# Kernel tuning notes

Hardware: AMD Instinct MI355X
Metric: run time of the kernel (lower is better)

## Reference

```python
import jax, jax.numpy as jnp
import numpy as np

B, L, I, O = 65536, 16, 256, 256


def setup_inputs() -> dict:
    key = jax.random.key(0)
    k1, k2, k3, k4 = jax.random.split(key, 4)
    lookups = jax.random.uniform(k1, (B, L), dtype=jnp.float32)
    values = jax.random.normal(k2, (B, I), dtype=jnp.float32)
    # glorot-style scale for the weight bank
    weights_lookup = jax.random.normal(k3, (L, I, O), dtype=jnp.float32) * (1.0 / np.sqrt(I))
    bias_lookup = jnp.zeros((L, O), dtype=jnp.float32)
    return {"lookups": lookups, "values": values,
            "weights_lookup": weights_lookup, "bias_lookup": bias_lookup}


def reference(lookups, values, weights_lookup, bias_lookup):
    # tf.einsum('...i,...l,lio->...o') with bias einsum('...l,lo->...o'),
    # activation = 'linear' (identity).
    # Efficient contraction order: per-token routed values (b,l,i) is avoided by
    # contracting values with the weight bank per expert, then combining with
    # routing weights — equivalent math, single einsum lets XLA pick the order.
    weighted = jnp.einsum('bi,bl,lio->bo', values, lookups, weights_lookup)
    biases = jnp.einsum('bl,lo->bo', lookups, bias_lookup)
    return weighted + biases
```

## Files before the change

kernel.cpp:

```cpp
#include <hip/hip_runtime.h>
#include <hip/hip_fp16.h>
#include <stdint.h>


#define B_TOK 65536
#define L_DIM 16
#define I_DIM 256
#define O_DIM 256
#define BM    256
#define THREADS 512

#define AOFF  65536
#define LKOFF 98304
#define LKS   20

typedef __attribute__((ext_vector_type(8))) _Float16 f16x8;
typedef __attribute__((ext_vector_type(4))) float f32x4;
typedef __attribute__((address_space(3))) void      lds_void_t;
typedef const __attribute__((address_space(1))) void gbl_void_t;

static __device__ __forceinline__ f16x8 scale8(f16x8 a, __half2 s) {
    union { f16x8 v; __half2 h[4]; } u; u.v = a;
#pragma unroll
    for (int q = 0; q < 4; ++q) u.h[q] = __hmul2(u.h[q], s);
    return u.v;
}

__global__ void prep_w(const float* __restrict__ W, const float* __restrict__ bias,
                       unsigned short* __restrict__ ws) {
    const int t  = blockIdx.x;
    const int o  = blockIdx.y * 32 + (threadIdx.x & 31);
    const int cp = threadIdx.x >> 5;
    const int c  = cp ^ (o & 7);
    uint32_t p[4];
    if (t < 64) {
        const int l = t & 15, ibase = (t >> 4) * 64;
        const float* src = W + ((size_t)l * I_DIM + ibase + c * 8) * O_DIM + o;
#pragma unroll
        for (int jp = 0; jp < 4; ++jp) {
            float a = src[(size_t)(2 * jp) * O_DIM];
            float b = src[(size_t)(2 * jp + 1) * O_DIM];
            p[jp] = __builtin_bit_cast(uint32_t, __floats2half2_rn(a, b));
        }
    } else if (c < 2) {
#pragma unroll
        for (int jp = 0; jp < 4; ++jp) {
            int kk = c * 8 + 2 * jp;
            float a = bias[(size_t)kk * O_DIM + o];
            float b = bias[(size_t)(kk + 1) * O_DIM + o];
            p[jp] = __builtin_bit_cast(uint32_t, __floats2half2_rn(a, b));
        }
    } else {
        p[0] = p[1] = p[2] = p[3] = 0u;
    }
    uint4 q = {p[0], p[1], p[2], p[3]};
    *(uint4*)((char*)ws + (size_t)t * 32768 + o * 128 + cp * 16) = q;
}

__launch_bounds__(THREADS, 2)
__global__ void md_gemm(const float* __restrict__ lookups,
                        const float* __restrict__ values,
                        const unsigned short* __restrict__ Wst,
                        float* __restrict__ out) {
    __shared__ char smem[118784];

    const int tid  = threadIdx.x;
    const int wid  = tid >> 6;
    const int lane = tid & 63;
    const int row0 = blockIdx.x * BM;

    const int r = tid >> 1;
    const int h = tid & 1;

    const int wm   = wid >> 2;
    const int wn   = wid & 3;
    const int arow = wm * 128 + (lane & 15);
    const int bcol = wn * 64  + (lane & 15);
    const int kkl  = (lane >> 4) * 8;

    f32x4 acc[8][4];
#pragma unroll
    for (int m = 0; m < 8; ++m)
#pragma unroll
        for (int n = 0; n < 4; ++n) acc[m][n] = (f32x4){0.f, 0.f, 0.f, 0.f};

    auto stageB = [&](int kt, int nb) {
        const char* src = (const char*)Wst + (size_t)kt * 32768 + wid * 1024 + lane * 16;
        char* dst = smem + nb * 32768 + wid * 1024;
#pragma unroll
        for (int s = 0; s < 4; ++s)
            __builtin_amdgcn_global_load_lds((gbl_void_t*)(src + s * 8192),
                                             (lds_void_t*)(dst + s * 8192), 16, 0, 0);
    };

    {
        const float4* lp = (const float4*)(lookups + (size_t)(row0 + r) * L_DIM + h * 8);
        float4 f0 = lp[0], f1 = lp[1];
        float* dst = (float*)(smem + LKOFF) + r * LKS + h * 8;
        *(float4*)dst = f0;
        *(float4*)(dst + 4) = f1;
    }
    stageB(0, 0);

    const float* lkp = (const float*)(smem + LKOFF);

    for (int cc = 0; cc < 4; ++cc) {
        {
            const float4* vp = (const float4*)(values + (size_t)(row0 + r) * I_DIM
                                               + cc * 64 + h * 32);
            uint32_t p[16];
#pragma unroll
            for (int j = 0; j < 8; ++j) {
                float4 f = vp[j];
                p[2 * j]     = __builtin_bit_cast(uint32_t, __floats2half2_rn(f.x, f.y));
                p[2 * j + 1] = __builtin_bit_cast(uint32_t, __floats2half2_rn(f.z, f.w));
            }
            char* ab = smem + AOFF;
#pragma unroll
            for (int w = 0; w < 4; ++w) {
                uint4 q = {p[4 * w], p[4 * w + 1], p[4 * w + 2], p[4 * w + 3]};
                *(uint4*)(ab + ((r * 128 + h * 64 + w * 16) ^ ((r & 7) << 4))) = q;
            }
        }
        __syncthreads();

        f16x8 afk0[8];
#pragma unroll
        for (int mt = 0; mt < 8; ++mt) {
            int row = arow + mt * 16;
            afk0[mt] = *(f16x8*)(smem + AOFF + ((row * 128 + kkl * 2) ^ ((row & 7) << 4)));
        }

        for (int l = 0; l < 16; ++l) {
            const int kt = cc * 16 + l;
            if (l != 0) {
                asm volatile("s_waitcnt vmcnt(0)\n\ts_barrier" ::: "memory");
            }
            __half2 lk2[8];
#pragma unroll
            for (int mt = 0; mt < 8; ++mt)
                lk2[mt] = __float2half2_rn(lkp[(arow + mt * 16) * LKS + l]);

            char* bbase = smem + (kt & 1) * 32768;
            f16x8 bfr[4];
#pragma unroll
            for (int nt = 0; nt < 4; ++nt) {
                int o = bcol + nt * 16;
                bfr[nt] = *(f16x8*)(bbase + ((o * 128 + kkl * 2) ^ ((o & 7) << 4)));
            }
#pragma unroll
            for (int mt = 0; mt < 8; ++mt) {
                f16x8 a = scale8(afk0[mt], lk2[mt]);
#pragma unroll
                for (int nt = 0; nt < 4; ++nt)
                    acc[mt][nt] = __builtin_amdgcn_mfma_f32_16x16x32_f16(
                        a, bfr[nt], acc[mt][nt], 0, 0, 0);
            }
#pragma unroll
            for (int nt = 0; nt < 4; ++nt) {
                int o = bcol + nt * 16;
                bfr[nt] = *(f16x8*)(bbase + ((o * 128 + 64 + kkl * 2) ^ ((o & 7) << 4)));
            }
#pragma unroll
            for (int mt = 0; mt < 8; ++mt) {
                int row = arow + mt * 16;
                f16x8 a1 = *(f16x8*)(smem + AOFF
                                     + ((row * 128 + 64 + kkl * 2) ^ ((row & 7) << 4)));
                a1 = scale8(a1, lk2[mt]);
#pragma unroll
                for (int nt = 0; nt < 4; ++nt)
                    acc[mt][nt] = __builtin_amdgcn_mfma_f32_16x16x32_f16(
                        a1, bfr[nt], acc[mt][nt], 0, 0, 0);
            }
            stageB(kt + 1, (kt + 1) & 1);
        }
        asm volatile("s_barrier" ::: "memory");
    }

    {
        uint32_t p[16];
#pragma unroll
        for (int j = 0; j < 16; ++j) p[j] = 0u;
        if (h == 0) {
            const float* lr = lkp + r * LKS;
#pragma unroll
            for (int j = 0; j < 8; ++j)
                p[j] = __builtin_bit_cast(uint32_t, __floats2half2_rn(lr[2 * j], lr[2 * j + 1]));
        }
        char* ab = smem + AOFF;
#pragma unroll
        for (int w = 0; w < 4; ++w) {
            uint4 q = {p[4 * w], p[4 * w + 1], p[4 * w + 2], p[4 * w + 3]};
            *(uint4*)(ab + ((r * 128 + h * 64 + w * 16) ^ ((r & 7) << 4))) = q;
        }
    }
    __syncthreads();
    {
        f16x8 bfr[4];
#pragma unroll
        for (int nt = 0; nt < 4; ++nt) {
            int o = bcol + nt * 16;
            bfr[nt] = *(f16x8*)(smem + ((o * 128 + kkl * 2) ^ ((o & 7) << 4)));
        }
#pragma unroll
        for (int mt = 0; mt < 8; ++mt) {
            int row = arow + mt * 16;
            f16x8 a0 = *(f16x8*)(smem + AOFF + ((row * 128 + kkl * 2) ^ ((row & 7) << 4)));
#pragma unroll
            for (int nt = 0; nt < 4; ++nt)
                acc[mt][nt] = __builtin_amdgcn_mfma_f32_16x16x32_f16(
                    a0, bfr[nt], acc[mt][nt], 0, 0, 0);
        }
    }

    const int orow = row0 + wm * 128 + (lane >> 4) * 4;
    const int ocol = wn * 64 + (lane & 15);
#pragma unroll
    for (int mt = 0; mt < 8; ++mt)
#pragma unroll
        for (int nt = 0; nt < 4; ++nt) {
#pragma unroll
            for (int j = 0; j < 4; ++j)
                out[(size_t)(orow + mt * 16 + j) * O_DIM + ocol + nt * 16] = acc[mt][nt][j];
        }
}

extern "C" void kernel_launch(void* const* d_in, const int* in_sizes, int n_in,
                              void* d_out, int out_size, void* d_ws, size_t ws_size,
                              hipStream_t stream) {
    const float* lookups = (const float*)d_in[0];
    const float* values  = (const float*)d_in[1];
    const float* W       = (const float*)d_in[2];
    const float* bias    = (const float*)d_in[3];
    unsigned short* Wst  = (unsigned short*)d_ws;

    prep_w<<<dim3(65, 8), dim3(256), 0, stream>>>(W, bias, Wst);
    md_gemm<<<dim3(B_TOK / BM), dim3(THREADS), 0, stream>>>(lookups, values, Wst,
                                                            (float*)d_out);
}
```

Before: 233.3 us.

## Triple-buffer weight tiles and interleave split async loads with MFMA phases

Replaces the double-buffered weight staging with a three-slot ring fetched two tiles ahead. Each tile's four async global-to-LDS loads are spread across four MFMA sub-phases, bracketed by barriers and raised wave priority. The per-chunk outer loop is flattened into one 64-step loop that reloads the activation slice at chunk boundaries, and the next routing scalar is prefetched into registers. The lookup row stride changes to 17 to reduce LDS bank conflicts. The cost is more LDS and more barriers per iteration, which may add synchronisation overhead.

```diff
diff --git a/kernel.cpp b/kernel.cpp
--- a/kernel.cpp
+++ b/kernel.cpp
@@ -10,14 +10,18 @@
 #define BM    256
 #define THREADS 512
 
-#define AOFF  65536
-#define LKOFF 98304
-#define LKS   20
+#define BOFS(i) ((i) * 32768)
+#define AOFF    98304
+#define LKOFF   131072
+#define LKS     17
 
 typedef __attribute__((ext_vector_type(8))) _Float16 f16x8;
 typedef __attribute__((ext_vector_type(4))) float f32x4;
 typedef __attribute__((address_space(3))) void      lds_void_t;
 typedef const __attribute__((address_space(1))) void gbl_void_t;
+
+#define SBAR  __builtin_amdgcn_s_barrier()
+#define SCHED __builtin_amdgcn_sched_barrier(0)
 
 static __device__ __forceinline__ f16x8 scale8(f16x8 a, __half2 s) {
     union { f16x8 v; __half2 h[4]; } u; u.v = a;
@@ -62,7 +66,7 @@
                         const float* __restrict__ values,
                         const unsigned short* __restrict__ Wst,
                         float* __restrict__ out) {
-    __shared__ char smem[118784];
+    __shared__ char smem[148480];
 
     const int tid  = threadIdx.x;
     const int wid  = tid >> 6;
@@ -78,139 +82,211 @@
     const int bcol = wn * 64  + (lane & 15);
     const int kkl  = (lane >> 4) * 8;
 
+    float* lkp = (float*)(smem + LKOFF);
+
     f32x4 acc[8][4];
 #pragma unroll
     for (int m = 0; m < 8; ++m)
 #pragma unroll
         for (int n = 0; n < 4; ++n) acc[m][n] = (f32x4){0.f, 0.f, 0.f, 0.f};
 
-    auto stageB = [&](int kt, int nb) {
-        const char* src = (const char*)Wst + (size_t)kt * 32768 + wid * 1024 + lane * 16;
-        char* dst = smem + nb * 32768 + wid * 1024;
-#pragma unroll
-        for (int s = 0; s < 4; ++s)
-            __builtin_amdgcn_global_load_lds((gbl_void_t*)(src + s * 8192),
-                                             (lds_void_t*)(dst + s * 8192), 16, 0, 0);
+    auto stage1 = [&](int g, int tb, int s) {
+        const char* src = (const char*)Wst + (size_t)g * 32768 + wid * 1024
+                          + s * 8192 + lane * 16;
+        char* dst = smem + BOFS(tb) + wid * 1024 + s * 8192;
+        __builtin_amdgcn_global_load_lds((gbl_void_t*)src, (lds_void_t*)dst, 16, 0, 0);
+    };
+
+    auto stageA = [&](int cc) {
+        const float4* vp = (const float4*)(values + (size_t)(row0 + r) * I_DIM
+                                           + cc * 64 + h * 32);
+        uint32_t p[16];
+#pragma unroll
+        for (int j = 0; j < 8; ++j) {
+            float4 f = vp[j];
+            p[2 * j]     = __builtin_bit_cast(uint32_t, __floats2half2_rn(f.x, f.y));
+            p[2 * j + 1] = __builtin_bit_cast(uint32_t, __floats2half2_rn(f.z, f.w));
+        }
+        char* ab = smem + AOFF;
+#pragma unroll
+        for (int w = 0; w < 4; ++w) {
+            uint4 q = {p[4 * w], p[4 * w + 1], p[4 * w + 2], p[4 * w + 3]};
+            *(uint4*)(ab + ((r * 128 + h * 64 + w * 16) ^ ((r & 7) << 4))) = q;
+        }
+    };
+
+    auto stageA_bias = [&]() {
+        uint32_t p[16];
+#pragma unroll
+        for (int j = 0; j < 16; ++j) p[j] = 0u;
+        if (h == 0) {
+            const float* lr = lkp + r * LKS;
+#pragma unroll
+            for (int j = 0; j < 8; ++j)
+                p[j] = __builtin_bit_cast(uint32_t,
+                        __floats2half2_rn(lr[2 * j], lr[2 * j + 1]));
+        }
+        char* ab = smem + AOFF;
+#pragma unroll
+        for (int w = 0; w < 4; ++w) {
+            uint4 q = {p[4 * w], p[4 * w + 1], p[4 * w + 2], p[4 * w + 3]};
+            *(uint4*)(ab + ((r * 128 + h * 64 + w * 16) ^ ((r & 7) << 4))) = q;
+        }
     };
 
     {
         const float4* lp = (const float4*)(lookups + (size_t)(row0 + r) * L_DIM + h * 8);
         float4 f0 = lp[0], f1 = lp[1];
-        float* dst = (float*)(smem + LKOFF) + r * LKS + h * 8;
-        *(float4*)dst = f0;
-        *(float4*)(dst + 4) = f1;
-    }
-    stageB(0, 0);
-
-    const float* lkp = (const float*)(smem + LKOFF);
-
-    for (int cc = 0; cc < 4; ++cc) {
+        float* dst = lkp + r * LKS + h * 8;
+        dst[0] = f0.x; dst[1] = f0.y; dst[2] = f0.z; dst[3] = f0.w;
+        dst[4] = f1.x; dst[5] = f1.y; dst[6] = f1.z; dst[7] = f1.w;
+    }
+#pragma unroll
+    for (int s = 0; s < 4; ++s) stage1(0, 0, s);
+#pragma unroll
+    for (int s = 0; s < 4; ++s) stage1(1, 1, s);
+    stageA(0);
+    __syncthreads();
+
+    f16x8 afk0[8];
+#pragma unroll
+    for (int mt = 0; mt < 8; ++mt) {
+        int row = arow + mt * 16;
+        afk0[mt] = *(f16x8*)(smem + AOFF + ((row * 128 + kkl * 2) ^ ((row & 7) << 4)));
+    }
+    float lknf[8];
+#pragma unroll
+    for (int mt = 0; mt < 8; ++mt) lknf[mt] = lkp[(arow + mt * 16) * LKS];
+
+    int bi = 0;
+    for (int kt = 0; kt < 64; ++kt) {
+        const int  tb       = (kt + 2) % 3;
+        const bool boundary = (kt & 15) == 15;
+        char* bbase = smem + BOFS(bi);
+
+        __half2 lk2[8];
+#pragma unroll
+        for (int mt = 0; mt < 8; ++mt) lk2[mt] = __float2half2_rn(lknf[mt]);
+
+        f16x8 bfr[4];
+#pragma unroll
+        for (int nt = 0; nt < 4; ++nt) {
+            int o = bcol + nt * 16;
+            bfr[nt] = *(f16x8*)(bbase + ((o * 128 + kkl * 2) ^ ((o & 7) << 4)));
+        }
+        if (kt <= 62) stage1(kt + 2, tb, 0);
+        SBAR; SCHED;
+        __builtin_amdgcn_s_setprio(1);
+#pragma unroll
+        for (int m = 0; m < 4; ++m) {
+            f16x8 a = scale8(afk0[m], lk2[m]);
+#pragma unroll
+            for (int nt = 0; nt < 4; ++nt)
+                acc[m][nt] = __builtin_amdgcn_mfma_f32_16x16x32_f16(a, bfr[nt],
+                                                                    acc[m][nt], 0, 0, 0);
+        }
+        __builtin_amdgcn_s_setprio(0);
+        SCHED; SBAR;
+
+        f16x8 a1lo[4];
+#pragma unroll
+        for (int m = 0; m < 4; ++m) {
+            int row = arow + m * 16;
+            a1lo[m] = *(f16x8*)(smem + AOFF
+                                + ((row * 128 + 64 + kkl * 2) ^ ((row & 7) << 4)));
+        }
+        if (kt <= 62) stage1(kt + 2, tb, 1);
+        SBAR; SCHED;
+        __builtin_amdgcn_s_setprio(1);
+#pragma unroll
+        for (int m = 4; m < 8; ++m) {
+            f16x8 a = scale8(afk0[m], lk2[m]);
+#pragma unroll
+            for (int nt = 0; nt < 4; ++nt)
+                acc[m][nt] = __builtin_amdgcn_mfma_f32_16x16x32_f16(a, bfr[nt],
+                                                                    acc[m][nt], 0, 0, 0);
+        }
+        __builtin_amdgcn_s_setprio(0);
+        SCHED; SBAR;
+
+        f16x8 b2[4];
+#pragma unroll
+        for (int nt = 0; nt < 4; ++nt) {
+            int o = bcol + nt * 16;
+            b2[nt] = *(f16x8*)(bbase + ((o * 128 + 64 + kkl * 2) ^ ((o & 7) << 4)));
+        }
+        f16x8 a1hi[4];
+#pragma unroll
+        for (int m = 0; m < 4; ++m) {
+            int row = arow + (m + 4) * 16;
+            a1hi[m] = *(f16x8*)(smem + AOFF
+                                + ((row * 128 + 64 + kkl * 2) ^ ((row & 7) << 4)));
+        }
+        if (kt <= 62) stage1(kt + 2, tb, 2);
+        SBAR; SCHED;
+        __builtin_amdgcn_s_setprio(1);
+#pragma unroll
+        for (int m = 0; m < 4; ++m) {
+            f16x8 a = scale8(a1lo[m], lk2[m]);
+#pragma unroll
+            for (int nt = 0; nt < 4; ++nt)
+                acc[m][nt] = __builtin_amdgcn_mfma_f32_16x16x32_f16(a, b2[nt],
+                                                                    acc[m][nt], 0, 0, 0);
+        }
+        __builtin_amdgcn_s_setprio(0);
+        SCHED; SBAR;
+
         {
-            const float4* vp = (const float4*)(values + (size_t)(row0 + r) * I_DIM
-                                               + cc * 64 + h * 32);
-            uint32_t p[16];
-#pragma unroll
-            for (int j = 0; j < 8; ++j) {
-                float4 f = vp[j];
-                p[2 * j]     = __builtin_bit_cast(uint32_t, __floats2half2_rn(f.x, f.y));
-                p[2 * j + 1] = __builtin_bit_cast(uint32_t, __floats2half2_rn(f.z, f.w));
-            }
-            char* ab = smem + AOFF;
-#pragma unroll
-            for (int w = 0; w < 4; ++w) {
-                uint4 q = {p[4 * w], p[4 * w + 1], p[4 * w + 2], p[4 * w + 3]};
-                *(uint4*)(ab + ((r * 128 + h * 64 + w * 16) ^ ((r & 7) << 4))) = q;
-            }
-        }
-        __syncthreads();
-
-        f16x8 afk0[8];
-#pragma unroll
-        for (int mt = 0; mt < 8; ++mt) {
-            int row = arow + mt * 16;
-            afk0[mt] = *(f16x8*)(smem + AOFF + ((row * 128 + kkl * 2) ^ ((row & 7) << 4)));
-        }
-
-        for (int l = 0; l < 16; ++l) {
-            const int kt = cc * 16 + l;
-            if (l != 0) {
-                asm volatile("s_waitcnt vmcnt(0)\n\ts_barrier" ::: "memory");
-            }
-            __half2 lk2[8];
+            int lnx = (kt + 1) & 15;
 #pragma unroll
             for (int mt = 0; mt < 8; ++mt)
-                lk2[mt] = __float2half2_rn(lkp[(arow + mt * 16) * LKS + l]);
-
-            char* bbase = smem + (kt & 1) * 32768;
-            f16x8 bfr[4];
-#pragma unroll
-            for (int nt = 0; nt < 4; ++nt) {
-                int o = bcol + nt * 16;
-                bfr[nt] = *(f16x8*)(bbase + ((o * 128 + kkl * 2) ^ ((o & 7) << 4)));
-            }
-#pragma unroll
-            for (int mt = 0; mt < 8; ++mt) {
-                f16x8 a = scale8(afk0[mt], lk2[mt]);
-#pragma unroll
-                for (int nt = 0; nt < 4; ++nt)
-                    acc[mt][nt] = __builtin_amdgcn_mfma_f32_16x16x32_f16(
-                        a, bfr[nt], acc[mt][nt], 0, 0, 0);
-            }
-#pragma unroll
-            for (int nt = 0; nt < 4; ++nt) {
-                int o = bcol + nt * 16;
-                bfr[nt] = *(f16x8*)(bbase + ((o * 128 + 64 + kkl * 2) ^ ((o & 7) << 4)));
-            }
+                lknf[mt] = lkp[(arow + mt * 16) * LKS + lnx];
+        }
+        if (kt <= 62) stage1(kt + 2, tb, 3);
+        SBAR; SCHED;
+        __builtin_amdgcn_s_setprio(1);
+#pragma unroll
+        for (int m = 0; m < 4; ++m) {
+            f16x8 a = scale8(a1hi[m], lk2[m + 4]);
+#pragma unroll
+            for (int nt = 0; nt < 4; ++nt)
+                acc[m + 4][nt] = __builtin_amdgcn_mfma_f32_16x16x32_f16(a, b2[nt],
+                                                                acc[m + 4][nt], 0, 0, 0);
+        }
+        __builtin_amdgcn_s_setprio(0);
+        SCHED;
+
+        if (!boundary) {
+            asm volatile("s_waitcnt vmcnt(4)" ::: "memory");
+            SBAR;
+        } else {
+            __syncthreads();
+            if (kt < 63) stageA((kt >> 4) + 1); else stageA_bias();
+            __syncthreads();
 #pragma unroll
             for (int mt = 0; mt < 8; ++mt) {
                 int row = arow + mt * 16;
-                f16x8 a1 = *(f16x8*)(smem + AOFF
-                                     + ((row * 128 + 64 + kkl * 2) ^ ((row & 7) << 4)));
-                a1 = scale8(a1, lk2[mt]);
-#pragma unroll
-                for (int nt = 0; nt < 4; ++nt)
-                    acc[mt][nt] = __builtin_amdgcn_mfma_f32_16x16x32_f16(
-                        a1, bfr[nt], acc[mt][nt], 0, 0, 0);
+                afk0[mt] = *(f16x8*)(smem + AOFF
+                                     + ((row * 128 + kkl * 2) ^ ((row & 7) << 4)));
             }
-            stageB(kt + 1, (kt + 1) & 1);
-        }
-        asm volatile("s_barrier" ::: "memory");
+        }
+        bi = (bi == 2) ? 0 : bi + 1;
     }
 
     {
-        uint32_t p[16];
-#pragma unroll
-        for (int j = 0; j < 16; ++j) p[j] = 0u;
-        if (h == 0) {
-            const float* lr = lkp + r * LKS;
-#pragma unroll
-            for (int j = 0; j < 8; ++j)
-                p[j] = __builtin_bit_cast(uint32_t, __floats2half2_rn(lr[2 * j], lr[2 * j + 1]));
-        }
-        char* ab = smem + AOFF;
-#pragma unroll
-        for (int w = 0; w < 4; ++w) {
-            uint4 q = {p[4 * w], p[4 * w + 1], p[4 * w + 2], p[4 * w + 3]};
-            *(uint4*)(ab + ((r * 128 + h * 64 + w * 16) ^ ((r & 7) << 4))) = q;
-        }
-    }
-    __syncthreads();
-    {
+        char* bbase = smem + BOFS(1);
         f16x8 bfr[4];
 #pragma unroll
         for (int nt = 0; nt < 4; ++nt) {
             int o = bcol + nt * 16;
-            bfr[nt] = *(f16x8*)(smem + ((o * 128 + kkl * 2) ^ ((o & 7) << 4)));
-        }
-#pragma unroll
-        for (int mt = 0; mt < 8; ++mt) {
-            int row = arow + mt * 16;
-            f16x8 a0 = *(f16x8*)(smem + AOFF + ((row * 128 + kkl * 2) ^ ((row & 7) << 4)));
-#pragma unroll
-            for (int nt = 0; nt < 4; ++nt)
-                acc[mt][nt] = __builtin_amdgcn_mfma_f32_16x16x32_f16(
-                    a0, bfr[nt], acc[mt][nt], 0, 0, 0);
-        }
+            bfr[nt] = *(f16x8*)(bbase + ((o * 128 + kkl * 2) ^ ((o & 7) << 4)));
+        }
+#pragma unroll
+        for (int m = 0; m < 8; ++m)
+#pragma unroll
+            for (int nt = 0; nt < 4; ++nt)
+                acc[m][nt] = __builtin_amdgcn_mfma_f32_16x16x32_f16(afk0[m], bfr[nt],
+                                                                    acc[m][nt], 0, 0, 0);
     }
 
     const int orow = row0 + wm * 128 + (lane >> 4) * 4;
```

Result: no change. 235.0 us (+0.8%).

## Restructure mixture GEMM main loop with early prefetch and precomputed LDS offsets

Applied to the files above, without the earlier changes.

Flattens the chunk/expert double loop into a single 64-step loop unrolled by two, with compile-time buffer indices. The next weight tile is now prefetched at the start of each step instead of the end. The lookup scalars are stored in LDS as pre-converted half2 values and loaded one step ahead, and all swizzled LDS offsets are computed once outside the loop. The goal is to hide global-to-LDS latency and cut address arithmetic and conversions in the inner loop. The cost is more register pressure, which could hurt at launch bounds of two blocks per CU. Issuing the prefetch into the other buffer before the barrier also depends on the end-of-step barrier for correctness.

```diff
diff --git a/kernel.cpp b/kernel.cpp
--- a/kernel.cpp
+++ b/kernel.cpp
@@ -10,9 +10,10 @@
 #define BM    256
 #define THREADS 512
 
-#define AOFF  65536
-#define LKOFF 98304
-#define LKS   20
+#define AOFF   65536
+#define LKOFF  98304
+#define LKROWB 72
+#define SMEMSZ 116736
 
 typedef __attribute__((ext_vector_type(8))) _Float16 f16x8;
 typedef __attribute__((ext_vector_type(4))) float f32x4;
@@ -62,7 +63,7 @@
                         const float* __restrict__ values,
                         const unsigned short* __restrict__ Wst,
                         float* __restrict__ out) {
-    __shared__ char smem[118784];
+    __shared__ char smem[SMEMSZ];
 
     const int tid  = threadIdx.x;
     const int wid  = tid >> 6;
@@ -78,139 +79,159 @@
     const int bcol = wn * 64  + (lane & 15);
     const int kkl  = (lane >> 4) * 8;
 
+    uint32_t oA[8], oA1[8], oB[4], oB1[4];
+#pragma unroll
+    for (int mt = 0; mt < 8; ++mt) {
+        int row = arow + mt * 16, swz = (row & 7) << 4, base = row * 128 + kkl * 2;
+        oA[mt]  = AOFF + (uint32_t)(base ^ swz);
+        oA1[mt] = AOFF + (uint32_t)((base + 64) ^ swz);
+    }
+#pragma unroll
+    for (int nt = 0; nt < 4; ++nt) {
+        int o = bcol + nt * 16, swz = (o & 7) << 4, base = o * 128 + kkl * 2;
+        oB[nt]  = (uint32_t)(base ^ swz);
+        oB1[nt] = (uint32_t)((base + 64) ^ swz);
+    }
+    const uint32_t oL = LKOFF + (uint32_t)arow * LKROWB;
+
     f32x4 acc[8][4];
 #pragma unroll
     for (int m = 0; m < 8; ++m)
 #pragma unroll
         for (int n = 0; n < 4; ++n) acc[m][n] = (f32x4){0.f, 0.f, 0.f, 0.f};
 
-    auto stageB = [&](int kt, int nb) {
-        const char* src = (const char*)Wst + (size_t)kt * 32768 + wid * 1024 + lane * 16;
-        char* dst = smem + nb * 32768 + wid * 1024;
+    auto stage1 = [&](int g, int nb) {
+        const char* src = (const char*)Wst + (size_t)g * 32768 + wid * 1024 + lane * 16;
 #pragma unroll
         for (int s = 0; s < 4; ++s)
-            __builtin_amdgcn_global_load_lds((gbl_void_t*)(src + s * 8192),
-                                             (lds_void_t*)(dst + s * 8192), 16, 0, 0);
+            __builtin_amdgcn_global_load_lds(
+                (gbl_void_t*)(src + s * 8192),
+                (lds_void_t*)&smem[nb * 32768 + wid * 1024 + s * 8192], 16, 0, 0);
+    };
+
+    auto stageA = [&](int cc) {
+        const float4* vp = (const float4*)(values + (size_t)(row0 + r) * I_DIM
+                                           + cc * 64 + h * 32);
+        uint32_t p[16];
+#pragma unroll
+        for (int j = 0; j < 8; ++j) {
+            float4 f = vp[j];
+            p[2 * j]     = __builtin_bit_cast(uint32_t, __floats2half2_rn(f.x, f.y));
+            p[2 * j + 1] = __builtin_bit_cast(uint32_t, __floats2half2_rn(f.z, f.w));
+        }
+#pragma unroll
+        for (int w = 0; w < 4; ++w) {
+            uint4 q = {p[4 * w], p[4 * w + 1], p[4 * w + 2], p[4 * w + 3]};
+            *(uint4*)&smem[AOFF + ((r * 128 + h * 64 + w * 16) ^ ((r & 7) << 4))] = q;
+        }
+    };
+
+    auto stageA_bias = [&]() {
+        uint32_t p[16];
+#pragma unroll
+        for (int j = 0; j < 16; ++j) p[j] = 0u;
+        if (h == 0) {
+            const __half* hp = (const __half*)&smem[LKOFF + r * LKROWB];
+#pragma unroll
+            for (int j = 0; j < 8; ++j) {
+                __half2 d; d.x = hp[4 * j]; d.y = hp[4 * j + 2];
+                p[j] = __builtin_bit_cast(uint32_t, d);
+            }
+        }
+#pragma unroll
+        for (int w = 0; w < 4; ++w) {
+            uint4 q = {p[4 * w], p[4 * w + 1], p[4 * w + 2], p[4 * w + 3]};
+            *(uint4*)&smem[AOFF + ((r * 128 + h * 64 + w * 16) ^ ((r & 7) << 4))] = q;
+        }
     };
 
     {
         const float4* lp = (const float4*)(lookups + (size_t)(row0 + r) * L_DIM + h * 8);
         float4 f0 = lp[0], f1 = lp[1];
-        float* dst = (float*)(smem + LKOFF) + r * LKS + h * 8;
-        *(float4*)dst = f0;
-        *(float4*)(dst + 4) = f1;
-    }
-    stageB(0, 0);
-
-    const float* lkp = (const float*)(smem + LKOFF);
-
-    for (int cc = 0; cc < 4; ++cc) {
+        float v[8] = {f0.x, f0.y, f0.z, f0.w, f1.x, f1.y, f1.z, f1.w};
+#pragma unroll
+        for (int j = 0; j < 8; ++j) {
+            __half hv = __float2half(v[j]);
+            __half2 d; d.x = hv; d.y = hv;
+            *(uint32_t*)&smem[LKOFF + r * LKROWB + (h * 8 + j) * 4] =
+                __builtin_bit_cast(uint32_t, d);
+        }
+    }
+    stage1(0, 0);
+    stageA(0);
+    __syncthreads();
+
+    f16x8 afk0[8];
+#pragma unroll
+    for (int mt = 0; mt < 8; ++mt)
+        afk0[mt] = *(const f16x8*)&smem[oA[mt]];
+
+    uint32_t lkA[8], lkB[8];
+#pragma unroll
+    for (int mt = 0; mt < 8; ++mt)
+        lkA[mt] = *(const uint32_t*)&smem[oL + mt * 1152];
+
+    auto body = [&](int kt, const int BUF, uint32_t (&cur)[8], uint32_t (&nxt)[8]) {
+        stage1(kt + 1, 1 - BUF);
         {
-            const float4* vp = (const float4*)(values + (size_t)(row0 + r) * I_DIM
-                                               + cc * 64 + h * 32);
-            uint32_t p[16];
-#pragma unroll
-            for (int j = 0; j < 8; ++j) {
-                float4 f = vp[j];
-                p[2 * j]     = __builtin_bit_cast(uint32_t, __floats2half2_rn(f.x, f.y));
-                p[2 * j + 1] = __builtin_bit_cast(uint32_t, __floats2half2_rn(f.z, f.w));
-            }
-            char* ab = smem + AOFF;
-#pragma unroll
-            for (int w = 0; w < 4; ++w) {
-                uint4 q = {p[4 * w], p[4 * w + 1], p[4 * w + 2], p[4 * w + 3]};
-                *(uint4*)(ab + ((r * 128 + h * 64 + w * 16) ^ ((r & 7) << 4))) = q;
-            }
-        }
-        __syncthreads();
-
-        f16x8 afk0[8];
-#pragma unroll
-        for (int mt = 0; mt < 8; ++mt) {
-            int row = arow + mt * 16;
-            afk0[mt] = *(f16x8*)(smem + AOFF + ((row * 128 + kkl * 2) ^ ((row & 7) << 4)));
-        }
-
-        for (int l = 0; l < 16; ++l) {
-            const int kt = cc * 16 + l;
-            if (l != 0) {
-                asm volatile("s_waitcnt vmcnt(0)\n\ts_barrier" ::: "memory");
-            }
-            __half2 lk2[8];
+            uint32_t ol = oL + (uint32_t)(((kt + 1) & 15) << 2);
 #pragma unroll
             for (int mt = 0; mt < 8; ++mt)
-                lk2[mt] = __float2half2_rn(lkp[(arow + mt * 16) * LKS + l]);
-
-            char* bbase = smem + (kt & 1) * 32768;
-            f16x8 bfr[4];
-#pragma unroll
-            for (int nt = 0; nt < 4; ++nt) {
-                int o = bcol + nt * 16;
-                bfr[nt] = *(f16x8*)(bbase + ((o * 128 + kkl * 2) ^ ((o & 7) << 4)));
-            }
-#pragma unroll
-            for (int mt = 0; mt < 8; ++mt) {
-                f16x8 a = scale8(afk0[mt], lk2[mt]);
-#pragma unroll
-                for (int nt = 0; nt < 4; ++nt)
-                    acc[mt][nt] = __builtin_amdgcn_mfma_f32_16x16x32_f16(
-                        a, bfr[nt], acc[mt][nt], 0, 0, 0);
-            }
-#pragma unroll
-            for (int nt = 0; nt < 4; ++nt) {
-                int o = bcol + nt * 16;
-                bfr[nt] = *(f16x8*)(bbase + ((o * 128 + 64 + kkl * 2) ^ ((o & 7) << 4)));
-            }
-#pragma unroll
-            for (int mt = 0; mt < 8; ++mt) {
-                int row = arow + mt * 16;
-                f16x8 a1 = *(f16x8*)(smem + AOFF
-                                     + ((row * 128 + 64 + kkl * 2) ^ ((row & 7) << 4)));
-                a1 = scale8(a1, lk2[mt]);
-#pragma unroll
-                for (int nt = 0; nt < 4; ++nt)
-                    acc[mt][nt] = __builtin_amdgcn_mfma_f32_16x16x32_f16(
-                        a1, bfr[nt], acc[mt][nt], 0, 0, 0);
-            }
-            stageB(kt + 1, (kt + 1) & 1);
-        }
-        asm volatile("s_barrier" ::: "memory");
+                nxt[mt] = *(const uint32_t*)&smem[ol + mt * 1152];
+        }
+        f16x8 b0[4];
+#pragma unroll
+        for (int nt = 0; nt < 4; ++nt)
+            b0[nt] = *(const f16x8*)&smem[oB[nt] + BUF * 32768];
+#pragma unroll
+        for (int m = 0; m < 8; ++m) {
+            f16x8 a = scale8(afk0[m], __builtin_bit_cast(__half2, cur[m]));
+#pragma unroll
+            for (int nt = 0; nt < 4; ++nt)
+                acc[m][nt] = __builtin_amdgcn_mfma_f32_16x16x32_f16(a, b0[nt],
+                                                                    acc[m][nt], 0, 0, 0);
+        }
+        f16x8 b1[4];
+#pragma unroll
+        for (int nt = 0; nt < 4; ++nt)
+            b1[nt] = *(const f16x8*)&smem[oB1[nt] + BUF * 32768];
+#pragma unroll
+        for (int m = 0; m < 8; ++m) {
+            f16x8 a1 = *(const f16x8*)&smem[oA1[m]];
+            a1 = scale8(a1, __builtin_bit_cast(__half2, cur[m]));
+#pragma unroll
+            for (int nt = 0; nt < 4; ++nt)
+                acc[m][nt] = __builtin_amdgcn_mfma_f32_16x16x32_f16(a1, b1[nt],
+                                                                    acc[m][nt], 0, 0, 0);
+        }
+        if ((kt & 15) == 15) {
+            __syncthreads();
+            if (kt < 63) stageA((kt >> 4) + 1); else stageA_bias();
+            __syncthreads();
+#pragma unroll
+            for (int mt = 0; mt < 8; ++mt)
+                afk0[mt] = *(const f16x8*)&smem[oA[mt]];
+        } else {
+            asm volatile("s_waitcnt vmcnt(0)\n\ts_barrier" ::: "memory");
+        }
+    };
+
+    for (int kt2 = 0; kt2 < 64; kt2 += 2) {
+        body(kt2,     0, lkA, lkB);
+        body(kt2 + 1, 1, lkB, lkA);
     }
 
     {
-        uint32_t p[16];
-#pragma unroll
-        for (int j = 0; j < 16; ++j) p[j] = 0u;
-        if (h == 0) {
-            const float* lr = lkp + r * LKS;
-#pragma unroll
-            for (int j = 0; j < 8; ++j)
-                p[j] = __builtin_bit_cast(uint32_t, __floats2half2_rn(lr[2 * j], lr[2 * j + 1]));
-        }
-        char* ab = smem + AOFF;
-#pragma unroll
-        for (int w = 0; w < 4; ++w) {
-            uint4 q = {p[4 * w], p[4 * w + 1], p[4 * w + 2], p[4 * w + 3]};
-            *(uint4*)(ab + ((r * 128 + h * 64 + w * 16) ^ ((r & 7) << 4))) = q;
-        }
-    }
-    __syncthreads();
-    {
-        f16x8 bfr[4];
-#pragma unroll
-        for (int nt = 0; nt < 4; ++nt) {
-            int o = bcol + nt * 16;
-            bfr[nt] = *(f16x8*)(smem + ((o * 128 + kkl * 2) ^ ((o & 7) << 4)));
-        }
-#pragma unroll
-        for (int mt = 0; mt < 8; ++mt) {
-            int row = arow + mt * 16;
-            f16x8 a0 = *(f16x8*)(smem + AOFF + ((row * 128 + kkl * 2) ^ ((row & 7) << 4)));
+        f16x8 b0[4];
+#pragma unroll
+        for (int nt = 0; nt < 4; ++nt)
+            b0[nt] = *(const f16x8*)&smem[oB[nt]];
+#pragma unroll
+        for (int m = 0; m < 8; ++m)
 #pragma unroll
             for (int nt = 0; nt < 4; ++nt)
-                acc[mt][nt] = __builtin_amdgcn_mfma_f32_16x16x32_f16(
-                    a0, bfr[nt], acc[mt][nt], 0, 0, 0);
-        }
+                acc[m][nt] = __builtin_amdgcn_mfma_f32_16x16x32_f16(afk0[m], b0[nt],
+                                                                    acc[m][nt], 0, 0, 0);
     }
 
     const int orow = row0 + wm * 128 + (lane >> 4) * 4;
```

After: 320.5 us. 1.37x slower.
